# Performance work log

Measured on AMD Instinct MI355X. Metric: run time of the kernel, lower is better.

Reference implementation:

```python
import math
import jax, jax.numpy as jnp
import numpy as np

B, T, C, H = 4, 1024, 1024, 16
HD = C // H
BLOCK = 1024


def setup_inputs() -> dict:
    key = jax.random.key(0)
    k0, k1, k2, k3 = jax.random.split(key, 4)
    x = jax.random.normal(k0, (B, T, C), dtype=jnp.float32)
    # torch Linear weight is (out, in); we store (in, out) and apply x @ W + b
    W_attn = jax.random.normal(k1, (C, 3 * C), dtype=jnp.float32) * 0.02
    b_attn = jnp.zeros((3 * C,), dtype=jnp.float32)
    W_proj = jax.random.normal(k2, (C, C), dtype=jnp.float32) * 0.02
    b_proj = jnp.zeros((C,), dtype=jnp.float32)
    # rel_pos_emb: (n_head, block_size, head_dim), std 0.02 (leading 1 dim dropped)
    rel_pos_emb = jax.random.normal(k3, (H, BLOCK, HD), dtype=jnp.float32) * 0.02
    return {"x": x, "W_attn": W_attn, "b_attn": b_attn,
            "W_proj": W_proj, "b_proj": b_proj, "rel_pos_emb": rel_pos_emb}


def reference(x, W_attn, b_attn, W_proj, b_proj, rel_pos_emb):
    Bx, Tx, Cx = x.shape
    qkv = x @ W_attn + b_attn                      # (B, T, 3C)
    q, k, v = jnp.split(qkv, 3, axis=2)
    q = q.reshape(Bx, Tx, H, HD).transpose(0, 2, 1, 3)   # (B, H, T, hd)
    k = k.reshape(Bx, Tx, H, HD).transpose(0, 2, 1, 3)
    v = v.reshape(Bx, Tx, H, HD).transpose(0, 2, 1, 3)

    att = jnp.einsum('bhid,bhjd->bhij', q, k)      # (B, H, T, T)

    # relative position score: pos[b,h,i,j] = sum_d E[h, clamp(i-j,0), d] * k[b,h,j,d]
    # compute P[b,h,r,j] = <E[h,r,:], k[b,h,j,:]> then gather r = clamp(i-j, 0)
    rng = jnp.arange(Tx)
    dist = jnp.clip(rng[:, None] - rng[None, :], 0, None)          # (T, T)
    P = jnp.einsum('hrd,bhjd->bhrj', rel_pos_emb[:, :Tx], k)       # (B, H, T, T)
    pos_score = jnp.take_along_axis(P, dist[None, None, :, :], axis=2)
    att = att + pos_score

    att = att * (1.0 / math.sqrt(HD))
    causal = jnp.tril(jnp.ones((Tx, Tx), dtype=bool))
    att = jnp.where(causal[None, None], att, -jnp.inf)
    att = jax.nn.softmax(att, axis=-1)
    # dropout p=0.0 -> identity
    y = jnp.einsum('bhij,bhjd->bhid', att, v)      # (B, H, T, hd)
    y = y.transpose(0, 2, 1, 3).reshape(Bx, Tx, Cx)
    return y @ W_proj + b_proj
```

## Files before the change

kernel.cpp:

```cpp
#include <hip/hip_runtime.h>


typedef __bf16 bf16x8 __attribute__((ext_vector_type(8)));
typedef float f32x4 __attribute__((ext_vector_type(4)));
typedef unsigned short ushort_t;

#define T_SEQ 1024
#define NHEAD 16
#define HDIM 64
#define PLANE 4194304
#define C1SCALE 0.1803368836f
#define SMAX 20.0f

__device__ __forceinline__ float bf2f(ushort_t h) {
    unsigned int u = ((unsigned int)h) << 16;
    float f; __builtin_memcpy(&f, &u, 4); return f;
}
__device__ __forceinline__ ushort_t f2bf(float f) {
    __bf16 h = (__bf16)f;
    ushort_t u; __builtin_memcpy(&u, &h, 2); return u;
}

__global__ __launch_bounds__(256) void sentinel_kernel(float* out, int n, float val) {
    const int i = blockIdx.x * 256 + threadIdx.x;
    if (i < n) out[i] = val;
}

__global__ __launch_bounds__(256) void prep(
    const float* __restrict__ x, ushort_t* __restrict__ x16,
    const float* __restrict__ E, ushort_t* __restrict__ E16,
    const float* __restrict__ Wa, ushort_t* __restrict__ WaT,
    const float* __restrict__ Wp, ushort_t* __restrict__ WpT)
{
    __shared__ ushort_t t[64][65];
    const int bid = blockIdx.x;
    if (bid < 5120) {
        const float* src; ushort_t* dst; int base; float sc;
        if (bid < 4096) { src = x; dst = x16; base = bid * 1024; sc = 1.0f; }
        else            { src = E; dst = E16; base = (bid - 4096) * 1024; sc = C1SCALE; }
        const int i = base + (int)threadIdx.x * 4;
        const float4 v = *reinterpret_cast<const float4*>(src + i);
        union { unsigned long long u; ushort_t s[4]; } o;
        o.s[0] = f2bf(v.x * sc); o.s[1] = f2bf(v.y * sc);
        o.s[2] = f2bf(v.z * sc); o.s[3] = f2bf(v.w * sc);
        *reinterpret_cast<unsigned long long*>(dst + i) = o.u;
        return;
    }
    const float* W; ushort_t* Wt; int Kdim, Ndim, n0, k0;
    if (bid < 5888) {
        const int r = bid - 5120;
        W = Wa; Wt = WaT; Kdim = 1024; Ndim = 3072;
        n0 = (r % 48) * 64; k0 = (r / 48) * 64;
    } else {
        const int r = bid - 5888;
        W = Wp; Wt = WpT; Kdim = 1024; Ndim = 1024;
        n0 = (r % 16) * 64; k0 = (r / 16) * 64;
    }
    const int cx = threadIdx.x & 63, ry = threadIdx.x >> 6;
#pragma unroll
    for (int i = 0; i < 16; i++) {
        const int r = ry + i * 4;
        t[r][cx] = f2bf(W[(size_t)(k0 + r) * Ndim + n0 + cx]);
    }
    __syncthreads();
#pragma unroll
    for (int i = 0; i < 16; i++) {
        const int r = ry + i * 4;
        Wt[(size_t)(n0 + r) * Kdim + k0 + cx] = t[cx][r];
    }
}

__global__ __launch_bounds__(256) void zero_ws(float* __restrict__ y32,
                                               float* __restrict__ den)
{
    const int bid = blockIdx.x;
    float4* p = (bid < 2048)
        ? reinterpret_cast<float4*>(y32) + (size_t)bid * 256 + threadIdx.x
        : reinterpret_cast<float4*>(den) + (size_t)(bid - 2048) * 256 + threadIdx.x;
    *p = (float4){0.f, 0.f, 0.f, 0.f};
}

__global__ __launch_bounds__(256) void norm_y(const float* __restrict__ y32,
                                              const float* __restrict__ den,
                                              ushort_t* __restrict__ y16)
{
    const int bid = blockIdx.x;
    const int b = bid >> 9, irel = bid & 511;
    const float4 v = reinterpret_cast<const float4*>(y32 + (size_t)bid * 1024)[threadIdx.x];
    const float inv = 1.0f / den[(size_t)bid * 16 + (threadIdx.x >> 4)];
    union { unsigned long long u; ushort_t s[4]; } o;
    o.s[0] = f2bf(v.x * inv); o.s[1] = f2bf(v.y * inv);
    o.s[2] = f2bf(v.z * inv); o.s[3] = f2bf(v.w * inv);
    reinterpret_cast<unsigned long long*>(
        y16 + ((size_t)(b * T_SEQ + 512 + irel)) * 1024)[threadIdx.x] = o.u;
}

template <int MODE, int BN>
__global__ __launch_bounds__(256) void gemm128(
    const ushort_t* __restrict__ A16, const ushort_t* __restrict__ Bt,
    const float* __restrict__ bias, void* __restrict__ out_,
    int Ndim, int Kdim)
{
    constexpr int NT = BN / 32;
    __shared__ __align__(16) ushort_t As[128 * 32];
    __shared__ __align__(16) ushort_t Bs[BN * 32];

    const int tid = threadIdx.x;
    const int w = tid >> 6;
    const int lane = tid & 63;
    const int l15 = lane & 15;
    const int quad = lane >> 4;
    const int m0 = blockIdx.y * 128, n0 = blockIdx.x * BN;
    const int wm = (w & 1) * 64, wn = (w >> 1) * (BN / 2);

    f32x4 acc[4][NT];
#pragma unroll
    for (int mt = 0; mt < 4; mt++)
#pragma unroll
        for (int nt = 0; nt < NT; nt++) acc[mt][nt] = (f32x4){0.f, 0.f, 0.f, 0.f};

    for (int kk = 0; kk < Kdim; kk += 32) {
        __syncthreads();
#pragma unroll
        for (int t = 0; t < 2; t++) {
            const int chunk = w * 128 + t * 64 + lane;
            const int row = chunk >> 2, kc = (chunk & 3) * 8;
            __builtin_amdgcn_global_load_lds(
                (const __attribute__((address_space(1))) void*)
                    (A16 + (size_t)(m0 + row) * Kdim + kk + kc),
                (__attribute__((address_space(3))) void*)
                    (As + (size_t)(w * 128 + t * 64) * 8), 16, 0, 0);
            if (BN == 128)
                __builtin_amdgcn_global_load_lds(
                    (const __attribute__((address_space(1))) void*)
                        (Bt + (size_t)(n0 + row) * Kdim + kk + kc),
                    (__attribute__((address_space(3))) void*)
                        (Bs + (size_t)(w * 128 + t * 64) * 8), 16, 0, 0);
        }
        if (BN == 64) {
            const int chunk = w * 64 + lane;
            const int row = chunk >> 2, kc = (chunk & 3) * 8;
            __builtin_amdgcn_global_load_lds(
                (const __attribute__((address_space(1))) void*)
                    (Bt + (size_t)(n0 + row) * Kdim + kk + kc),
                (__attribute__((address_space(3))) void*)
                    (Bs + (size_t)(w * 64) * 8), 16, 0, 0);
        }
        __syncthreads();

        bf16x8 af[4], bf[NT];
#pragma unroll
        for (int mt = 0; mt < 4; mt++)
            af[mt] = *reinterpret_cast<const bf16x8*>(&As[(wm + mt * 16 + l15) * 32 + quad * 8]);
#pragma unroll
        for (int nt = 0; nt < NT; nt++)
            bf[nt] = *reinterpret_cast<const bf16x8*>(&Bs[(wn + nt * 16 + l15) * 32 + quad * 8]);
#pragma unroll
        for (int mt = 0; mt < 4; mt++)
#pragma unroll
            for (int nt = 0; nt < NT; nt++)
                acc[mt][nt] = __builtin_amdgcn_mfma_f32_16x16x32_bf16(
                    af[mt], bf[nt], acc[mt][nt], 0, 0, 0);
    }

#pragma unroll
    for (int mt = 0; mt < 4; mt++)
#pragma unroll
        for (int nt = 0; nt < NT; nt++) {
            const int n = n0 + wn + nt * 16 + l15;
            const float bv = bias[n];
#pragma unroll
            for (int r = 0; r < 4; r++) {
                const int m = m0 + wm + mt * 16 + quad * 4 + r;
                const float val = acc[mt][nt][r] + bv;
                if (MODE == 0) {
                    ushort_t* ws = (ushort_t*)out_;
                    const int which = n >> 10;
                    const int cc = n & 1023;
                    const int h = cc >> 6, d = cc & 63;
                    const int bb = m >> 10, t = m & 1023;
                    if (which == 2) {
                        ws[2 * PLANE + ((size_t)(bb * NHEAD + h) * HDIM + d) * T_SEQ + t] = f2bf(val);
                    } else {
                        const float sv = (which == 0) ? val * C1SCALE : val;
                        ws[(size_t)which * PLANE +
                           ((size_t)(bb * NHEAD + h) * T_SEQ + t) * HDIM + d] = f2bf(sv);
                    }
                } else {
                    ((float*)out_)[(size_t)m * Ndim + n] = val;
                }
            }
        }
}

__global__ __launch_bounds__(256) void flash_attn(
    const ushort_t* __restrict__ qp, const ushort_t* __restrict__ kp,
    const ushort_t* __restrict__ vTp, const ushort_t* __restrict__ E16,
    ushort_t* __restrict__ y16, float* __restrict__ y32,
    float* __restrict__ den)
{
    __shared__ __align__(16) ushort_t Ks[64 * 64];
    __shared__ __align__(16) ushort_t Vt[64 * 64];
    __shared__ __align__(16) ushort_t Es[128 * 64];
    __shared__ __align__(16) ushort_t Ps[64 * 64];

    static const signed char TBL_IT[24] =
        {15,15,14, 7,14,13,13,12, 6,12,11,11,10, 5,10, 9, 9, 8, 4, 8, 3, 2, 1, 0};
    static const signed char TBL_HF[24] =
        { 0, 1, 0, 2, 1, 0, 1, 0, 2, 1, 0, 1, 0, 2, 1, 0, 1, 0, 2, 1, 2, 2, 2, 2};

    const int bh = blockIdx.x;
    const int h = bh & (NHEAD - 1);
    const int b = bh >> 4;
    const int by = blockIdx.y;
    const int it = TBL_IT[by];
    const int hf = TBL_HF[by];
    const int ntile = it + 1;
    const int jb = (hf == 1) ? ((it + 2) >> 1) : 0;
    const int je = (hf == 0) ? ((it + 2) >> 1) : ntile;

    const int tid = threadIdx.x;
    const int w = tid >> 6;
    const int lane = tid & 63;
    const int l15 = lane & 15;
    const int quad = lane >> 4;

    const size_t base = (size_t)bh * T_SEQ * HDIM;
    const ushort_t* Eh = E16 + (size_t)h * T_SEQ * HDIM;
    const ushort_t* vTb = vTp + (size_t)bh * 65536;

    const int kswz = (l15 & 7) << 3;
    const int jswz = quad << 4;

    const int srow = lane >> 3;
    const int scc  = lane & 7;

    bf16x8 ones;
#pragma unroll
    for (int i = 0; i < 8; i++) ones[i] = (__bf16)1.0f;

    const int i0 = it * 64;

    bf16x8 qf[2];
    {
        const ushort_t* qrow = qp + base + (size_t)(i0 + w * 16 + l15) * HDIM;
        qf[0] = *reinterpret_cast<const bf16x8*>(qrow + quad * 8);
        qf[1] = *reinterpret_cast<const bf16x8*>(qrow + 32 + quad * 8);
    }

    f32x4 o[4], o5;
#pragma unroll
    for (int dt = 0; dt < 4; dt++) o[dt] = (f32x4){0.f, 0.f, 0.f, 0.f};
    o5 = (f32x4){0.f, 0.f, 0.f, 0.f};

    for (int jt = jb; jt < je; ++jt) {
        const int j0 = jt * 64;
        const int d0 = i0 - j0;
        __syncthreads();
        {
#pragma unroll
            for (int t = 0; t < 2; t++) {
                const int r0 = w * 16 + t * 8;
                const int row = r0 + srow;
                const int sx = (scc ^ (row & 7)) << 3;
                __builtin_amdgcn_global_load_lds(
                    (const __attribute__((address_space(1))) void*)
                        (kp + base + (size_t)(j0 + row) * HDIM + sx),
                    (__attribute__((address_space(3))) void*)(&Ks[r0 * 64]),
                    16, 0, 0);
                __builtin_amdgcn_global_load_lds(
                    (const __attribute__((address_space(1))) void*)
                        (vTb + (size_t)row * T_SEQ + j0 + sx),
                    (__attribute__((address_space(3))) void*)(&Vt[r0 * 64]),
                    16, 0, 0);
            }
#pragma unroll
            for (int t = 0; t < 4; t++) {
                const int r0 = w * 32 + t * 8;
                const int row = r0 + srow;
                int g = d0 - 64 + row;
                g = g < 0 ? 0 : (g > 1023 ? 1023 : g);
                const int sx = (scc ^ (row & 7)) << 3;
                __builtin_amdgcn_global_load_lds(
                    (const __attribute__((address_space(1))) void*)
                        (Eh + (size_t)g * HDIM + sx),
                    (__attribute__((address_space(3))) void*)(&Es[r0 * 64]),
                    16, 0, 0);
            }
        }
        __syncthreads();

        f32x4 s[4], pb[2][4];
#pragma unroll
        for (int nt = 0; nt < 4; nt++) {
            s[nt] = (f32x4){0.f, 0.f, 0.f, 0.f};
            pb[0][nt] = (f32x4){0.f, 0.f, 0.f, 0.f};
            pb[1][nt] = (f32x4){0.f, 0.f, 0.f, 0.f};
        }
        __builtin_amdgcn_s_setprio(1);
#pragma unroll
        for (int ks = 0; ks < 2; ks++) {
            const int ko = ks * 32 + quad * 8;
            const bf16x8 ae0 = *reinterpret_cast<const bf16x8*>(&Es[(w * 32 + l15) * 64 + (ko ^ kswz)]);
            const bf16x8 ae1 = *reinterpret_cast<const bf16x8*>(&Es[(w * 32 + 16 + l15) * 64 + (ko ^ kswz)]);
#pragma unroll
            for (int nt = 0; nt < 4; nt++) {
                const bf16x8 bk = *reinterpret_cast<const bf16x8*>(&Ks[(nt * 16 + l15) * 64 + (ko ^ kswz)]);
                s[nt] = __builtin_amdgcn_mfma_f32_16x16x32_bf16(qf[ks], bk, s[nt], 0, 0, 0);
                pb[0][nt] = __builtin_amdgcn_mfma_f32_16x16x32_bf16(ae0, bk, pb[0][nt], 0, 0, 0);
                pb[1][nt] = __builtin_amdgcn_mfma_f32_16x16x32_bf16(ae1, bk, pb[1][nt], 0, 0, 0);
            }
        }
        __builtin_amdgcn_s_setprio(0);
#pragma unroll
        for (int mf = 0; mf < 2; mf++)
#pragma unroll
            for (int nt = 0; nt < 4; nt++) {
                const int jl = nt * 16 + l15;
#pragma unroll
                for (int r = 0; r < 4; r++) {
                    const int br = w * 32 + mf * 16 + quad * 4 + r;
                    const int il_t = br - 64 + jl;
                    if ((unsigned)il_t < 64u)
                        Ps[il_t * 64 + (jl ^ (((il_t >> 2) & 3) << 4))] = f2bf(pb[mf][nt][r]);
                }
            }
        __syncthreads();

        float pv[4][4];
        const int il0 = w * 16 + quad * 4;
        if (j0 < i0) {
#pragma unroll
            for (int nt = 0; nt < 4; nt++) {
                const int jl = nt * 16 + l15;
#pragma unroll
                for (int r = 0; r < 4; r++) {
                    const float sv = s[nt][r] + bf2f(Ps[(il0 + r) * 64 + (jl ^ jswz)]);
                    pv[nt][r] = exp2f(sv - SMAX);
                }
            }
        } else {
#pragma unroll
            for (int nt = 0; nt < 4; nt++) {
                const int jl = nt * 16 + l15;
#pragma unroll
                for (int r = 0; r < 4; r++) {
                    const int il = il0 + r;
                    float sv = s[nt][r] + bf2f(Ps[il * 64 + (jl ^ jswz)]);
                    if (jl > il) sv = -3e38f;
                    pv[nt][r] = exp2f(sv - SMAX);
                }
            }
        }
#pragma unroll
        for (int nt = 0; nt < 4; nt++)
#pragma unroll
            for (int r = 0; r < 4; r++) {
                const int rr = w * 16 + quad * 4 + r;
                Ks[rr * 64 + ((nt * 16 + l15) ^ ((rr & 7) << 3))] = f2bf(pv[nt][r]);
            }

        __builtin_amdgcn_s_setprio(1);
#pragma unroll
        for (int ks = 0; ks < 2; ks++) {
            const int ko = ks * 32 + quad * 8;
            const bf16x8 ap = *reinterpret_cast<const bf16x8*>(&Ks[(w * 16 + l15) * 64 + (ko ^ kswz)]);
#pragma unroll
            for (int dt = 0; dt < 4; dt++) {
                const bf16x8 bv = *reinterpret_cast<const bf16x8*>(&Vt[(dt * 16 + l15) * 64 + (ko ^ kswz)]);
                o[dt] = __builtin_amdgcn_mfma_f32_16x16x32_bf16(ap, bv, o[dt], 0, 0, 0);
            }
            o5 = __builtin_amdgcn_mfma_f32_16x16x32_bf16(ap, ones, o5, 0, 0, 0);
        }
        __builtin_amdgcn_s_setprio(0);
    }

    if (hf == 2) {
        float inv[4];
#pragma unroll
        for (int r = 0; r < 4; r++) inv[r] = 1.0f / o5[r];
#pragma unroll
        for (int dt = 0; dt < 4; dt++)
#pragma unroll
            for (int r = 0; r < 4; r++) {
                const int il = w * 16 + quad * 4 + r;
                const int d = dt * 16 + l15;
                y16[((size_t)(b * T_SEQ + i0 + il)) * 1024 + h * 64 + d] =
                    f2bf(o[dt][r] * inv[r]);
            }
    } else {
        const int rb = b * 512 + (i0 - 512);
#pragma unroll
        for (int dt = 0; dt < 4; dt++)
#pragma unroll
            for (int r = 0; r < 4; r++) {
                const int il = w * 16 + quad * 4 + r;
                const int d = dt * 16 + l15;
                atomicAdd(&y32[((size_t)(rb + il)) * 1024 + h * 64 + d], o[dt][r]);
            }
        if (l15 == 0) {
#pragma unroll
            for (int r = 0; r < 4; r++) {
                const int il = w * 16 + quad * 4 + r;
                atomicAdd(&den[(size_t)(rb + il) * 16 + h], o5[r]);
            }
        }
    }
}

extern "C" void kernel_launch(void* const* d_in, const int* in_sizes, int n_in,
                              void* d_out, int out_size, void* d_ws, size_t ws_size,
                              hipStream_t stream) {
    float* out = (float*)d_out;

    const void* x = nullptr; const void* Wa = nullptr; const void* ba = nullptr;
    const void* Wp = nullptr; const void* bp = nullptr; const void* E = nullptr;
    int anomaly = 0;
    if (n_in != 6) {
        anomaly = 2;
    } else {
        int c1M = 0;
        for (int i = 0; i < 6; i++) {
            const int s = in_sizes[i];
            if      (s == 4194304) x  = d_in[i];
            else if (s == 3145728) Wa = d_in[i];
            else if (s == 3072)    ba = d_in[i];
            else if (s == 1024)    bp = d_in[i];
            else if (s == 1048576) { if (c1M == 0) Wp = d_in[i]; else E = d_in[i]; c1M++; }
            else anomaly = 1;
        }
        if (!x || !Wa || !ba || !Wp || !bp || !E || c1M != 2) anomaly = 1;
    }
    if (!anomaly && out_size != 4194304) anomaly = 3;
    if (!anomaly && ws_size < (size_t)52428800) anomaly = 4;
    if (anomaly) {
        sentinel_kernel<<<(out_size + 255) / 256, 256, 0, stream>>>(out, out_size, 1000.0f * anomaly);
        return;
    }

    ushort_t* ws   = (ushort_t*)d_ws;
    ushort_t* qp   = ws;
    ushort_t* kp   = ws + (size_t)PLANE;
    ushort_t* vTp  = ws + (size_t)2 * PLANE;
    ushort_t* y16  = ws + (size_t)3 * PLANE;
    ushort_t* x16  = ws + (size_t)4 * PLANE;
    ushort_t* WaT  = ws + (size_t)5 * PLANE;
    ushort_t* WpT  = WaT + (size_t)3145728;
    ushort_t* E16  = WpT + (size_t)1048576;

    float* y32 = (float*)x16;
    float* den = (float*)WaT;

    prep<<<6144, 256, 0, stream>>>((const float*)x, x16, (const float*)E, E16,
                                   (const float*)Wa, WaT, (const float*)Wp, WpT);

    gemm128<0, 128><<<dim3(24, 32), 256, 0, stream>>>(x16, WaT, (const float*)ba, (void*)ws, 3072, 1024);

    zero_ws<<<2080, 256, 0, stream>>>(y32, den);

    flash_attn<<<dim3(64, 24), 256, 0, stream>>>(qp, kp, vTp, E16, y16, y32, den);

    norm_y<<<2048, 256, 0, stream>>>(y32, den, y16);

    gemm128<1, 64><<<dim3(16, 32), 256, 0, stream>>>(y16, WpT, (const float*)bp, (void*)out, 1024, 1024);
}
```

Baseline: 227.2 us.

## Rebalance causal attention work: split only top tiles, pair short query tiles

Reworks the flash-attention grid from 24 to 16 blocks per batch-head. Only the four longest query tiles are split across two blocks with atomic accumulation; middle tiles run whole, and the shortest tiles are paired so one block processes two query tiles in sequence. This shrinks the atomic-accumulated region and the zeroing and normalization passes to 256 rows per batch. It also cuts the block count and tail imbalance, at the cost of a somewhat larger maximum per-block workload.

Result: faster. 215.3 us (-5.2%).

```diff
diff --git a/kernel.cpp b/kernel.cpp
--- a/kernel.cpp
+++ b/kernel.cpp
@@ -74,9 +74,9 @@
                                                float* __restrict__ den)
 {
     const int bid = blockIdx.x;
-    float4* p = (bid < 2048)
+    float4* p = (bid < 1024)
         ? reinterpret_cast<float4*>(y32) + (size_t)bid * 256 + threadIdx.x
-        : reinterpret_cast<float4*>(den) + (size_t)(bid - 2048) * 256 + threadIdx.x;
+        : reinterpret_cast<float4*>(den) + (size_t)(bid - 1024) * 256 + threadIdx.x;
     *p = (float4){0.f, 0.f, 0.f, 0.f};
 }
 
@@ -85,14 +85,14 @@
                                               ushort_t* __restrict__ y16)
 {
     const int bid = blockIdx.x;
-    const int b = bid >> 9, irel = bid & 511;
+    const int b = bid >> 8, irel = bid & 255;
     const float4 v = reinterpret_cast<const float4*>(y32 + (size_t)bid * 1024)[threadIdx.x];
     const float inv = 1.0f / den[(size_t)bid * 16 + (threadIdx.x >> 4)];
     union { unsigned long long u; ushort_t s[4]; } o;
     o.s[0] = f2bf(v.x * inv); o.s[1] = f2bf(v.y * inv);
     o.s[2] = f2bf(v.z * inv); o.s[3] = f2bf(v.w * inv);
     reinterpret_cast<unsigned long long*>(
-        y16 + ((size_t)(b * T_SEQ + 512 + irel)) * 1024)[threadIdx.x] = o.u;
+        y16 + ((size_t)(b * T_SEQ + 768 + irel)) * 1024)[threadIdx.x] = o.u;
 }
 
 template <int MODE, int BN>
@@ -204,20 +204,24 @@
     __shared__ __align__(16) ushort_t Es[128 * 64];
     __shared__ __align__(16) ushort_t Ps[64 * 64];
 
-    static const signed char TBL_IT[24] =
-        {15,15,14, 7,14,13,13,12, 6,12,11,11,10, 5,10, 9, 9, 8, 4, 8, 3, 2, 1, 0};
-    static const signed char TBL_HF[24] =
-        { 0, 1, 0, 2, 1, 0, 1, 0, 2, 1, 0, 1, 0, 2, 1, 0, 1, 0, 2, 1, 2, 2, 2, 2};
-
     const int bh = blockIdx.x;
     const int h = bh & (NHEAD - 1);
     const int b = bh >> 4;
     const int by = blockIdx.y;
-    const int it = TBL_IT[by];
-    const int hf = TBL_HF[by];
-    const int ntile = it + 1;
-    const int jb = (hf == 1) ? ((it + 2) >> 1) : 0;
-    const int je = (hf == 0) ? ((it + 2) >> 1) : ntile;
+
+    int itA, jbA, jeA, itB = -1;
+    bool atomA = false;
+    if (by < 8) {
+        itA = 15 - (by >> 1);
+        const int nt = itA + 1, h1 = (nt + 1) >> 1;
+        jbA = (by & 1) ? h1 : 0;
+        jeA = (by & 1) ? nt : h1;
+        atomA = true;
+    } else if (by < 12) {
+        itA = 19 - by; jbA = 0; jeA = itA + 1;
+    } else {
+        itA = 19 - by; jbA = 0; jeA = itA + 1; itB = by - 12;
+    }
 
     const int tid = threadIdx.x;
     const int w = tid >> 6;
@@ -239,170 +243,180 @@
 #pragma unroll
     for (int i = 0; i < 8; i++) ones[i] = (__bf16)1.0f;
 
-    const int i0 = it * 64;
-
-    bf16x8 qf[2];
-    {
-        const ushort_t* qrow = qp + base + (size_t)(i0 + w * 16 + l15) * HDIM;
-        qf[0] = *reinterpret_cast<const bf16x8*>(qrow + quad * 8);
-        qf[1] = *reinterpret_cast<const bf16x8*>(qrow + 32 + quad * 8);
-    }
-
-    f32x4 o[4], o5;
-#pragma unroll
-    for (int dt = 0; dt < 4; dt++) o[dt] = (f32x4){0.f, 0.f, 0.f, 0.f};
-    o5 = (f32x4){0.f, 0.f, 0.f, 0.f};
-
-    for (int jt = jb; jt < je; ++jt) {
-        const int j0 = jt * 64;
-        const int d0 = i0 - j0;
-        __syncthreads();
+#pragma unroll 1
+    for (int job = 0; job < 2; ++job) {
+        int it, jb, je;
+        bool atp;
+        if (job == 0) { it = itA; jb = jbA; je = jeA; atp = atomA; }
+        else {
+            if (itB < 0) break;
+            it = itB; jb = 0; je = itB + 1; atp = false;
+        }
+        const int i0 = it * 64;
+
+        bf16x8 qf[2];
         {
-#pragma unroll
-            for (int t = 0; t < 2; t++) {
-                const int r0 = w * 16 + t * 8;
-                const int row = r0 + srow;
-                const int sx = (scc ^ (row & 7)) << 3;
-                __builtin_amdgcn_global_load_lds(
-                    (const __attribute__((address_space(1))) void*)
-                        (kp + base + (size_t)(j0 + row) * HDIM + sx),
-                    (__attribute__((address_space(3))) void*)(&Ks[r0 * 64]),
-                    16, 0, 0);
-                __builtin_amdgcn_global_load_lds(
-                    (const __attribute__((address_space(1))) void*)
-                        (vTb + (size_t)row * T_SEQ + j0 + sx),
-                    (__attribute__((address_space(3))) void*)(&Vt[r0 * 64]),
-                    16, 0, 0);
-            }
-#pragma unroll
-            for (int t = 0; t < 4; t++) {
-                const int r0 = w * 32 + t * 8;
-                const int row = r0 + srow;
-                int g = d0 - 64 + row;
-                g = g < 0 ? 0 : (g > 1023 ? 1023 : g);
-                const int sx = (scc ^ (row & 7)) << 3;
-                __builtin_amdgcn_global_load_lds(
-                    (const __attribute__((address_space(1))) void*)
-                        (Eh + (size_t)g * HDIM + sx),
-                    (__attribute__((address_space(3))) void*)(&Es[r0 * 64]),
-                    16, 0, 0);
-            }
-        }
-        __syncthreads();
-
-        f32x4 s[4], pb[2][4];
-#pragma unroll
-        for (int nt = 0; nt < 4; nt++) {
-            s[nt] = (f32x4){0.f, 0.f, 0.f, 0.f};
-            pb[0][nt] = (f32x4){0.f, 0.f, 0.f, 0.f};
-            pb[1][nt] = (f32x4){0.f, 0.f, 0.f, 0.f};
-        }
-        __builtin_amdgcn_s_setprio(1);
-#pragma unroll
-        for (int ks = 0; ks < 2; ks++) {
-            const int ko = ks * 32 + quad * 8;
-            const bf16x8 ae0 = *reinterpret_cast<const bf16x8*>(&Es[(w * 32 + l15) * 64 + (ko ^ kswz)]);
-            const bf16x8 ae1 = *reinterpret_cast<const bf16x8*>(&Es[(w * 32 + 16 + l15) * 64 + (ko ^ kswz)]);
+            const ushort_t* qrow = qp + base + (size_t)(i0 + w * 16 + l15) * HDIM;
+            qf[0] = *reinterpret_cast<const bf16x8*>(qrow + quad * 8);
+            qf[1] = *reinterpret_cast<const bf16x8*>(qrow + 32 + quad * 8);
+        }
+
+        f32x4 o[4], o5;
+#pragma unroll
+        for (int dt = 0; dt < 4; dt++) o[dt] = (f32x4){0.f, 0.f, 0.f, 0.f};
+        o5 = (f32x4){0.f, 0.f, 0.f, 0.f};
+
+        for (int jt = jb; jt < je; ++jt) {
+            const int j0 = jt * 64;
+            const int d0 = i0 - j0;
+            __syncthreads();
+            {
+#pragma unroll
+                for (int t = 0; t < 2; t++) {
+                    const int r0 = w * 16 + t * 8;
+                    const int row = r0 + srow;
+                    const int sx = (scc ^ (row & 7)) << 3;
+                    __builtin_amdgcn_global_load_lds(
+                        (const __attribute__((address_space(1))) void*)
+                            (kp + base + (size_t)(j0 + row) * HDIM + sx),
+                        (__attribute__((address_space(3))) void*)(&Ks[r0 * 64]),
+                        16, 0, 0);
+                    __builtin_amdgcn_global_load_lds(
+                        (const __attribute__((address_space(1))) void*)
+                            (vTb + (size_t)row * T_SEQ + j0 + sx),
+                        (__attribute__((address_space(3))) void*)(&Vt[r0 * 64]),
+                        16, 0, 0);
+                }
+#pragma unroll
+                for (int t = 0; t < 4; t++) {
+                    const int r0 = w * 32 + t * 8;
+                    const int row = r0 + srow;
+                    int g = d0 - 64 + row;
+                    g = g < 0 ? 0 : (g > 1023 ? 1023 : g);
+                    const int sx = (scc ^ (row & 7)) << 3;
+                    __builtin_amdgcn_global_load_lds(
+                        (const __attribute__((address_space(1))) void*)
+                            (Eh + (size_t)g * HDIM + sx),
+                        (__attribute__((address_space(3))) void*)(&Es[r0 * 64]),
+                        16, 0, 0);
+                }
+            }
+            __syncthreads();
+
+            f32x4 s[4], pb[2][4];
 #pragma unroll
             for (int nt = 0; nt < 4; nt++) {
-                const bf16x8 bk = *reinterpret_cast<const bf16x8*>(&Ks[(nt * 16 + l15) * 64 + (ko ^ kswz)]);
-                s[nt] = __builtin_amdgcn_mfma_f32_16x16x32_bf16(qf[ks], bk, s[nt], 0, 0, 0);
-                pb[0][nt] = __builtin_amdgcn_mfma_f32_16x16x32_bf16(ae0, bk, pb[0][nt], 0, 0, 0);
-                pb[1][nt] = __builtin_amdgcn_mfma_f32_16x16x32_bf16(ae1, bk, pb[1][nt], 0, 0, 0);
-            }
-        }
-        __builtin_amdgcn_s_setprio(0);
-#pragma unroll
-        for (int mf = 0; mf < 2; mf++)
-#pragma unroll
-            for (int nt = 0; nt < 4; nt++) {
-                const int jl = nt * 16 + l15;
+                s[nt] = (f32x4){0.f, 0.f, 0.f, 0.f};
+                pb[0][nt] = (f32x4){0.f, 0.f, 0.f, 0.f};
+                pb[1][nt] = (f32x4){0.f, 0.f, 0.f, 0.f};
+            }
+            __builtin_amdgcn_s_setprio(1);
+#pragma unroll
+            for (int ks = 0; ks < 2; ks++) {
+                const int ko = ks * 32 + quad * 8;
+                const bf16x8 ae0 = *reinterpret_cast<const bf16x8*>(&Es[(w * 32 + l15) * 64 + (ko ^ kswz)]);
+                const bf16x8 ae1 = *reinterpret_cast<const bf16x8*>(&Es[(w * 32 + 16 + l15) * 64 + (ko ^ kswz)]);
+#pragma unroll
+                for (int nt = 0; nt < 4; nt++) {
+                    const bf16x8 bk = *reinterpret_cast<const bf16x8*>(&Ks[(nt * 16 + l15) * 64 + (ko ^ kswz)]);
+                    s[nt] = __builtin_amdgcn_mfma_f32_16x16x32_bf16(qf[ks], bk, s[nt], 0, 0, 0);
+                    pb[0][nt] = __builtin_amdgcn_mfma_f32_16x16x32_bf16(ae0, bk, pb[0][nt], 0, 0, 0);
+                    pb[1][nt] = __builtin_amdgcn_mfma_f32_16x16x32_bf16(ae1, bk, pb[1][nt], 0, 0, 0);
+                }
+            }
+            __builtin_amdgcn_s_setprio(0);
+#pragma unroll
+            for (int mf = 0; mf < 2; mf++)
+#pragma unroll
+                for (int nt = 0; nt < 4; nt++) {
+                    const int jl = nt * 16 + l15;
+#pragma unroll
+                    for (int r = 0; r < 4; r++) {
+                        const int br = w * 32 + mf * 16 + quad * 4 + r;
+                        const int il_t = br - 64 + jl;
+                        if ((unsigned)il_t < 64u)
+                            Ps[il_t * 64 + (jl ^ (((il_t >> 2) & 3) << 4))] = f2bf(pb[mf][nt][r]);
+                    }
+                }
+            __syncthreads();
+
+            float pv[4][4];
+            const int il0 = w * 16 + quad * 4;
+            if (j0 < i0) {
+#pragma unroll
+                for (int nt = 0; nt < 4; nt++) {
+                    const int jl = nt * 16 + l15;
+#pragma unroll
+                    for (int r = 0; r < 4; r++) {
+                        const float sv = s[nt][r] + bf2f(Ps[(il0 + r) * 64 + (jl ^ jswz)]);
+                        pv[nt][r] = exp2f(sv - SMAX);
+                    }
+                }
+            } else {
+#pragma unroll
+                for (int nt = 0; nt < 4; nt++) {
+                    const int jl = nt * 16 + l15;
+#pragma unroll
+                    for (int r = 0; r < 4; r++) {
+                        const int il = il0 + r;
+                        float sv = s[nt][r] + bf2f(Ps[il * 64 + (jl ^ jswz)]);
+                        if (jl > il) sv = -3e38f;
+                        pv[nt][r] = exp2f(sv - SMAX);
+                    }
+                }
+            }
+#pragma unroll
+            for (int nt = 0; nt < 4; nt++)
 #pragma unroll
                 for (int r = 0; r < 4; r++) {
-                    const int br = w * 32 + mf * 16 + quad * 4 + r;
-                    const int il_t = br - 64 + jl;
-                    if ((unsigned)il_t < 64u)
-                        Ps[il_t * 64 + (jl ^ (((il_t >> 2) & 3) << 4))] = f2bf(pb[mf][nt][r]);
-                }
-            }
-        __syncthreads();
-
-        float pv[4][4];
-        const int il0 = w * 16 + quad * 4;
-        if (j0 < i0) {
-#pragma unroll
-            for (int nt = 0; nt < 4; nt++) {
-                const int jl = nt * 16 + l15;
+                    const int rr = w * 16 + quad * 4 + r;
+                    Ks[rr * 64 + ((nt * 16 + l15) ^ ((rr & 7) << 3))] = f2bf(pv[nt][r]);
+                }
+
+            __builtin_amdgcn_s_setprio(1);
+#pragma unroll
+            for (int ks = 0; ks < 2; ks++) {
+                const int ko = ks * 32 + quad * 8;
+                const bf16x8 ap = *reinterpret_cast<const bf16x8*>(&Ks[(w * 16 + l15) * 64 + (ko ^ kswz)]);
+#pragma unroll
+                for (int dt = 0; dt < 4; dt++) {
+                    const bf16x8 bv = *reinterpret_cast<const bf16x8*>(&Vt[(dt * 16 + l15) * 64 + (ko ^ kswz)]);
+                    o[dt] = __builtin_amdgcn_mfma_f32_16x16x32_bf16(ap, bv, o[dt], 0, 0, 0);
+                }
+                o5 = __builtin_amdgcn_mfma_f32_16x16x32_bf16(ap, ones, o5, 0, 0, 0);
+            }
+            __builtin_amdgcn_s_setprio(0);
+        }
+
+        if (!atp) {
+            float inv[4];
+#pragma unroll
+            for (int r = 0; r < 4; r++) inv[r] = 1.0f / o5[r];
+#pragma unroll
+            for (int dt = 0; dt < 4; dt++)
 #pragma unroll
                 for (int r = 0; r < 4; r++) {
-                    const float sv = s[nt][r] + bf2f(Ps[(il0 + r) * 64 + (jl ^ jswz)]);
-                    pv[nt][r] = exp2f(sv - SMAX);
-                }
-            }
+                    const int il = w * 16 + quad * 4 + r;
+                    const int d = dt * 16 + l15;
+                    y16[((size_t)(b * T_SEQ + i0 + il)) * 1024 + h * 64 + d] =
+                        f2bf(o[dt][r] * inv[r]);
+                }
         } else {
-#pragma unroll
-            for (int nt = 0; nt < 4; nt++) {
-                const int jl = nt * 16 + l15;
+            const int rb = b * 256 + (i0 - 768);
+#pragma unroll
+            for (int dt = 0; dt < 4; dt++)
 #pragma unroll
                 for (int r = 0; r < 4; r++) {
-                    const int il = il0 + r;
-                    float sv = s[nt][r] + bf2f(Ps[il * 64 + (jl ^ jswz)]);
-                    if (jl > il) sv = -3e38f;
-                    pv[nt][r] = exp2f(sv - SMAX);
-                }
-            }
-        }
-#pragma unroll
-        for (int nt = 0; nt < 4; nt++)
-#pragma unroll
-            for (int r = 0; r < 4; r++) {
-                const int rr = w * 16 + quad * 4 + r;
-                Ks[rr * 64 + ((nt * 16 + l15) ^ ((rr & 7) << 3))] = f2bf(pv[nt][r]);
-            }
-
-        __builtin_amdgcn_s_setprio(1);
-#pragma unroll
-        for (int ks = 0; ks < 2; ks++) {
-            const int ko = ks * 32 + quad * 8;
-            const bf16x8 ap = *reinterpret_cast<const bf16x8*>(&Ks[(w * 16 + l15) * 64 + (ko ^ kswz)]);
-#pragma unroll
-            for (int dt = 0; dt < 4; dt++) {
-                const bf16x8 bv = *reinterpret_cast<const bf16x8*>(&Vt[(dt * 16 + l15) * 64 + (ko ^ kswz)]);
-                o[dt] = __builtin_amdgcn_mfma_f32_16x16x32_bf16(ap, bv, o[dt], 0, 0, 0);
-            }
-            o5 = __builtin_amdgcn_mfma_f32_16x16x32_bf16(ap, ones, o5, 0, 0, 0);
-        }
-        __builtin_amdgcn_s_setprio(0);
-    }
-
-    if (hf == 2) {
-        float inv[4];
-#pragma unroll
-        for (int r = 0; r < 4; r++) inv[r] = 1.0f / o5[r];
-#pragma unroll
-        for (int dt = 0; dt < 4; dt++)
-#pragma unroll
-            for (int r = 0; r < 4; r++) {
-                const int il = w * 16 + quad * 4 + r;
-                const int d = dt * 16 + l15;
-                y16[((size_t)(b * T_SEQ + i0 + il)) * 1024 + h * 64 + d] =
-                    f2bf(o[dt][r] * inv[r]);
-            }
-    } else {
-        const int rb = b * 512 + (i0 - 512);
-#pragma unroll
-        for (int dt = 0; dt < 4; dt++)
-#pragma unroll
-            for (int r = 0; r < 4; r++) {
-                const int il = w * 16 + quad * 4 + r;
-                const int d = dt * 16 + l15;
-                atomicAdd(&y32[((size_t)(rb + il)) * 1024 + h * 64 + d], o[dt][r]);
-            }
-        if (l15 == 0) {
-#pragma unroll
-            for (int r = 0; r < 4; r++) {
-                const int il = w * 16 + quad * 4 + r;
-                atomicAdd(&den[(size_t)(rb + il) * 16 + h], o5[r]);
+                    const int il = w * 16 + quad * 4 + r;
+                    const int d = dt * 16 + l15;
+                    atomicAdd(&y32[((size_t)(rb + il)) * 1024 + h * 64 + d], o[dt][r]);
+                }
+            if (l15 == 0) {
+#pragma unroll
+                for (int r = 0; r < 4; r++) {
+                    const int il = w * 16 + quad * 4 + r;
+                    atomicAdd(&den[(size_t)(rb + il) * 16 + h], o5[r]);
+                }
             }
         }
     }
@@ -456,11 +470,11 @@
 
     gemm128<0, 128><<<dim3(24, 32), 256, 0, stream>>>(x16, WaT, (const float*)ba, (void*)ws, 3072, 1024);
 
-    zero_ws<<<2080, 256, 0, stream>>>(y32, den);
-
-    flash_attn<<<dim3(64, 24), 256, 0, stream>>>(qp, kp, vTp, E16, y16, y32, den);
-
-    norm_y<<<2048, 256, 0, stream>>>(y32, den, y16);
+    zero_ws<<<1040, 256, 0, stream>>>(y32, den);
+
+    flash_attn<<<dim3(64, 16), 256, 0, stream>>>(qp, kp, vTp, E16, y16, y32, den);
+
+    norm_y<<<1024, 256, 0, stream>>>(y32, den, y16);
 
     gemm128<1, 64><<<dim3(16, 32), 256, 0, stream>>>(y16, WpT, (const float*)bp, (void*)out, 1024, 1024);
 }
```
